# Kernel optimization log

Hardware: AMD Instinct MI355X
Metric: run time of the kernel (lower is better)

## Reference

```python
import jax, jax.numpy as jnp
import numpy as np

D_MODEL = 1024
HIDDEN = 1024
N_EXPERTS = 8
TOP_K = 2
BATCH, SEQ = 2, 2048
N_TOKENS = BATCH * SEQ


def setup_inputs() -> dict:
    key = jax.random.key(0)
    ks = jax.random.split(key, 6)
    x = jax.random.normal(ks[0], (BATCH, SEQ, D_MODEL), dtype=jnp.float32)
    expert_weights = jax.random.uniform(ks[1], (N_TOKENS, TOP_K), dtype=jnp.float32)
    expert_indices = jax.random.randint(ks[2], (N_TOKENS, TOP_K), 0, N_EXPERTS, dtype=jnp.int32)
    s_in = 1.0 / np.sqrt(D_MODEL)
    s_hid = 1.0 / np.sqrt(HIDDEN)
    w1 = jax.random.normal(ks[3], (N_EXPERTS, D_MODEL, HIDDEN), dtype=jnp.float32) * s_in
    w3 = jax.random.normal(ks[4], (N_EXPERTS, D_MODEL, HIDDEN), dtype=jnp.float32) * s_in
    w2 = jax.random.normal(ks[5], (N_EXPERTS, HIDDEN, D_MODEL), dtype=jnp.float32) * s_hid
    return {"x": x, "expert_weights": expert_weights, "expert_indices": expert_indices,
            "w1": w1, "w3": w3, "w2": w2}


def reference(x, expert_weights, expert_indices, w1, w3, w2):
    """Dropless MoE MLP (forward_once path): for each token t,
    out[t] = sum_k expert_weights[t,k] * SwiGLU_{expert_indices[t,k]}(x[t]).
    Also returns batch_size_per_expert (histogram of routed assignments).
    """
    d = x.shape[-1]
    xf = x.reshape(-1, d)                                  # [N, d]
    E = w1.shape[0]
    # combine[t, e] = sum over top-k slots routed to expert e of their weight
    onehot = jax.nn.one_hot(expert_indices, E, dtype=xf.dtype)       # [N, K, E]
    combine = jnp.einsum("nk,nke->ne", expert_weights, onehot)      # [N, E]
    out = jnp.zeros_like(xf)
    for e in range(E):  # fixed small loop over experts
        h = jax.nn.silu(xf @ w1[e]) * (xf @ w3[e])          # [N, H]
        out = out + combine[:, e:e + 1] * (h @ w2[e])       # [N, d]
    batch_size_per_expert = jnp.zeros((E,), dtype=jnp.int32).at[
        expert_indices.reshape(-1)].add(1)
    return out.reshape(x.shape), batch_size_per_expert
```

## Files before the change

### kernel.cpp

```cpp
#include <hip/hip_runtime.h>
#include <cstdint>

#define D 1024
#define N_TOKENS 4096
#define N_SLOTS 8192
#define NEXP 8
#define NKT 16
#define MAXT 80

typedef float f32x4 __attribute__((ext_vector_type(4)));
typedef __bf16 bf16x8 __attribute__((ext_vector_type(8)));
typedef __attribute__((address_space(3))) uint32_t lds_u32;
typedef __attribute__((address_space(1))) const uint32_t glb_u32;

__device__ __forceinline__ void gload_lds16(const void* g, void* l) {
  __builtin_amdgcn_global_load_lds((glb_u32*)g, (lds_u32*)l, 16, 0, 0);
}

__device__ __forceinline__ ushort f2bf(float f) {
  union { float f; uint32_t u; } c; c.f = f;
  uint32_t u = c.u;
  return (ushort)((u + 0x7FFFu + ((u >> 16) & 1u)) >> 16);
}

__device__ __forceinline__ float bf2f(ushort u) {
  union { uint32_t u; float f; } c; c.u = (uint32_t)u << 16;
  return c.f;
}

__device__ __forceinline__ bf16x8 lds_frag(const ushort* base, int row, int s) {
  return *(const bf16x8*)((const char*)base + row * 128 + ((s ^ (row & 7)) * 16));
}

__global__ void prep_k(const float* __restrict__ x, const int* __restrict__ ei,
                       const float* __restrict__ ew,
                       const float* __restrict__ w1, const float* __restrict__ w3,
                       float* __restrict__ hist_out, int* __restrict__ meta,
                       int* __restrict__ tok, int* __restrict__ smap,
                       ushort* __restrict__ Xbf, ushort* __restrict__ w13t) {
  int bid = blockIdx.x, t = threadIdx.x;
  if (bid == 0) {
    __shared__ int cmat[256][8];
    __shared__ int off[NEXP + 1];
#pragma unroll
    for (int e = 0; e < NEXP; e++) cmat[t][e] = 0;
    int base = t * 32;
#pragma unroll 4
    for (int j = 0; j < 32; j++) cmat[t][ei[base + j]]++;
    __syncthreads();
    if (t < NEXP) {
      int run = 0;
      for (int i = 0; i < 256; i++) { int v = cmat[i][t]; cmat[i][t] = run; run += v; }
      meta[8 + t] = run;
    }
    __syncthreads();
    if (t == 0) {
      int s = 0;
      for (int e = 0; e < NEXP; e++) { off[e] = s; s += meta[8 + e]; }
      off[NEXP] = s;
      int nt = 0;
      for (int e = 0; e < NEXP; e++)
        for (int r = off[e]; r < off[e + 1]; r += 128)
          if (nt < MAXT) {
            meta[16 + nt] = e;
            meta[96 + nt] = r;
            int re = off[e + 1]; if (r + 128 < re) re = r + 128;
            meta[176 + nt] = re;
            nt++;
          }
      meta[0] = nt;
      for (int e = 0; e < NEXP; e++) hist_out[e] = (float)meta[8 + e];
    }
    __syncthreads();
#pragma unroll 4
    for (int j = 0; j < 32; j++) {
      int slot = base + j;
      int e = ei[slot];
      int p = off[e] + cmat[t][e]++;
      tok[p] = slot >> 1;
      smap[slot] = p;
    }
  } else if (bid <= 256) {
    int cb = bid - 1;
    const float4* xs = (const float4*)x + (size_t)cb * 4096;
    ushort4* xd = (ushort4*)Xbf + (size_t)cb * 4096;
#pragma unroll
    for (int i = 0; i < 16; i++) {
      float4 v = xs[i * 256 + t];
      ushort4 o;
      o.x = f2bf(v.x); o.y = f2bf(v.y); o.z = f2bf(v.z); o.w = f2bf(v.w);
      xd[i * 256 + t] = o;
    }
  } else {
    int wb = bid - 257;
    int z = wb >> 8, rem = wb & 255;
    int kb = rem >> 4, nb = rem & 15;
    int which = z >> 3, e = z & 7;
    const float* src = (which == 0 ? w1 : w3) + (size_t)e * D * D;
    ushort* dst = w13t + (size_t)e * 2048 * D;
    __shared__ ushort tile[64][72];
    int k0 = kb * 64, n0 = nb * 64;
    int r = t >> 4, c = t & 15;
#pragma unroll
    for (int rep = 0; rep < 4; rep++) {
      int krow = rep * 16 + r;
      float4 v = *(const float4*)(src + (size_t)(k0 + krow) * D + n0 + c * 4);
      tile[krow][c * 4 + 0] = f2bf(v.x);
      tile[krow][c * 4 + 1] = f2bf(v.y);
      tile[krow][c * 4 + 2] = f2bf(v.z);
      tile[krow][c * 4 + 3] = f2bf(v.w);
    }
    __syncthreads();
#pragma unroll
    for (int rep = 0; rep < 4; rep++) {
      int lr = rep * 16 + r;
      int nrow = n0 + lr;
      ushort4 o;
      o.x = tile[c * 4 + 0][lr];
      o.y = tile[c * 4 + 1][lr];
      o.z = tile[c * 4 + 2][lr];
      o.w = tile[c * 4 + 3][lr];
      int crow = ((nrow >> 4) << 5) + ((which == 1) ? 16 : 0) + (nrow & 15);
      *(ushort4*)(dst + (size_t)crow * D + k0 + c * 4) = o;
    }
  }
}

#define STAGE_TILE(sAb, sBb, kb_) do {                                        \
  int kb = (kb_);                                                             \
  _Pragma("unroll")                                                           \
  for (int i = 0; i < 4; i++) {                                               \
    gload_lds16(gA + arow[i] + kb + phys[i],                                  \
                (char*)(sAb) + (i * 256 + tid) * 16);                         \
    gload_lds16(gB + (size_t)brow[i] * 2048 + kb + phys[i],                   \
                (char*)(sBb) + (i * 256 + tid) * 16);                         \
  } } while (0)

__global__ __launch_bounds__(256, 2) void gemm1_k(
    const ushort* __restrict__ Xbf, const ushort* __restrict__ W13t,
    ushort* __restrict__ H, const int* __restrict__ tok,
    const int* __restrict__ meta,
    const float* __restrict__ w2, ushort* __restrict__ W2t) {
  __shared__ ushort sA[2][128 * 64];
  __shared__ ushort sB[2][128 * 64];
  int tm = blockIdx.y;
  int tid = threadIdx.x;

  if (tm >= MAXT) {
    int e = tm - MAXT;
    const float* src = w2 + (size_t)e * D * D;
    ushort* dst = W2t + (size_t)e * D * D;
    ushort (*tile)[72] = (ushort(*)[72]) & sA[0][0];
    int kb = blockIdx.x;
    int r = tid >> 4, c = tid & 15;
    int k0 = kb * 64;
    for (int nb = 0; nb < 16; nb++) {
      int n0 = nb * 64;
      __syncthreads();
#pragma unroll
      for (int rep = 0; rep < 4; rep++) {
        int krow = rep * 16 + r;
        float4 v = *(const float4*)(src + (size_t)(k0 + krow) * D + n0 + c * 4);
        tile[krow][c * 4 + 0] = f2bf(v.x);
        tile[krow][c * 4 + 1] = f2bf(v.y);
        tile[krow][c * 4 + 2] = f2bf(v.z);
        tile[krow][c * 4 + 3] = f2bf(v.w);
      }
      __syncthreads();
#pragma unroll
      for (int rep = 0; rep < 4; rep++) {
        int lr = rep * 16 + r;
        ushort4 o;
        o.x = tile[c * 4 + 0][lr];
        o.y = tile[c * 4 + 1][lr];
        o.z = tile[c * 4 + 2][lr];
        o.w = tile[c * 4 + 3][lr];
        *(ushort4*)(dst + (size_t)(n0 + lr) * D + k0 + c * 4) = o;
      }
    }
    return;
  }
  if (tm >= meta[0]) return;

  int e = meta[16 + tm], r0 = meta[96 + tm], rend = meta[176 + tm];
  int n0i = blockIdx.x * 128;
  int lane = tid & 63, wid = tid >> 6;
  int wm = wid >> 1, wn = wid & 1;

  const char* gA = (const char*)Xbf;
  const char* gB = (const char*)(W13t + (size_t)e * 2048 * D);

  int prow = tid >> 3, pslot = tid & 7;
  size_t arow[4];
  int brow[4], phys[4];
#pragma unroll
  for (int i = 0; i < 4; i++) {
    int row = i * 32 + prow;
    int gr = r0 + row; if (gr > N_SLOTS - 1) gr = N_SLOTS - 1;
    arow[i] = (size_t)tok[gr] * 2048;
    brow[i] = n0i + row;
    phys[i] = (pslot ^ (row & 7)) * 16;
  }

  f32x4 acc[4][4] = {};

  STAGE_TILE(&sA[0][0], &sB[0][0], 0);
  int cur = 0;
  for (int kt = 0; kt < NKT; kt++) {
    if (kt + 1 < NKT) {
      STAGE_TILE(&sA[cur ^ 1][0], &sB[cur ^ 1][0], (kt + 1) * 128);
      asm volatile("s_waitcnt vmcnt(8)" ::: "memory");
    } else {
      asm volatile("s_waitcnt vmcnt(0)" ::: "memory");
    }
    __builtin_amdgcn_s_barrier();
#pragma unroll
    for (int kk = 0; kk < 2; kk++) {
      int s = kk * 4 + (lane >> 4);
      bf16x8 a[4], b[4];
#pragma unroll
      for (int mf = 0; mf < 4; mf++)
        a[mf] = lds_frag(&sA[cur][0], wm * 64 + mf * 16 + (lane & 15), s);
#pragma unroll
      for (int nf = 0; nf < 4; nf++)
        b[nf] = lds_frag(&sB[cur][0], wn * 64 + nf * 16 + (lane & 15), s);
#pragma unroll
      for (int mf = 0; mf < 4; mf++)
#pragma unroll
        for (int nf = 0; nf < 4; nf++)
          acc[mf][nf] = __builtin_amdgcn_mfma_f32_16x16x32_bf16(a[mf], b[nf], acc[mf][nf], 0, 0, 0);
    }
    __builtin_amdgcn_s_barrier();
    __builtin_amdgcn_sched_barrier(0);
    cur ^= 1;
  }

  int cb = (n0i >> 1) + wn * 32 + (lane & 15);
#pragma unroll
  for (int mf = 0; mf < 4; mf++)
#pragma unroll
    for (int v = 0; v < 4; v++) {
      int r = r0 + wm * 64 + mf * 16 + (lane >> 4) * 4 + v;
      if (r >= rend) continue;
#pragma unroll
      for (int p = 0; p < 2; p++) {
        float g = acc[mf][2 * p][v], u = acc[mf][2 * p + 1][v];
        float hv = g / (1.f + __expf(-g)) * u;
        H[(size_t)r * D + cb + p * 16] = f2bf(hv);
      }
    }
}

__global__ __launch_bounds__(256, 2) void gemm2_k(
    const ushort* __restrict__ Hm, const ushort* __restrict__ W2t,
    ushort* __restrict__ Y, const int* __restrict__ meta) {
  __shared__ ushort sA[2][128 * 64];
  __shared__ ushort sB[2][128 * 64];
  int tm = blockIdx.y;
  if (tm >= meta[0]) return;
  int e = meta[16 + tm], r0 = meta[96 + tm], rend = meta[176 + tm];
  int n0 = blockIdx.x * 128;
  int tid = threadIdx.x, lane = tid & 63, wid = tid >> 6;
  int wm = wid >> 1, wn = wid & 1;

  const char* gA = (const char*)Hm;
  const char* gB = (const char*)(W2t + (size_t)e * D * D);

  int prow = tid >> 3, pslot = tid & 7;
  size_t arow[4];
  int brow[4], phys[4];
#pragma unroll
  for (int i = 0; i < 4; i++) {
    int row = i * 32 + prow;
    int gr = r0 + row; if (gr > N_SLOTS - 1) gr = N_SLOTS - 1;
    arow[i] = (size_t)gr * 2048;
    brow[i] = n0 + row;
    phys[i] = (pslot ^ (row & 7)) * 16;
  }

  f32x4 acc[4][4] = {};

  STAGE_TILE(&sA[0][0], &sB[0][0], 0);
  int cur = 0;
  for (int kt = 0; kt < NKT; kt++) {
    if (kt + 1 < NKT) {
      STAGE_TILE(&sA[cur ^ 1][0], &sB[cur ^ 1][0], (kt + 1) * 128);
      asm volatile("s_waitcnt vmcnt(8)" ::: "memory");
    } else {
      asm volatile("s_waitcnt vmcnt(0)" ::: "memory");
    }
    __builtin_amdgcn_s_barrier();
#pragma unroll
    for (int kk = 0; kk < 2; kk++) {
      int s = kk * 4 + (lane >> 4);
      bf16x8 a[4], b[4];
#pragma unroll
      for (int mf = 0; mf < 4; mf++)
        a[mf] = lds_frag(&sA[cur][0], wm * 64 + mf * 16 + (lane & 15), s);
#pragma unroll
      for (int nf = 0; nf < 4; nf++)
        b[nf] = lds_frag(&sB[cur][0], wn * 64 + nf * 16 + (lane & 15), s);
#pragma unroll
      for (int mf = 0; mf < 4; mf++)
#pragma unroll
        for (int nf = 0; nf < 4; nf++)
          acc[mf][nf] = __builtin_amdgcn_mfma_f32_16x16x32_bf16(a[mf], b[nf], acc[mf][nf], 0, 0, 0);
    }
    __builtin_amdgcn_s_barrier();
    __builtin_amdgcn_sched_barrier(0);
    cur ^= 1;
  }

#pragma unroll
  for (int mf = 0; mf < 4; mf++)
#pragma unroll
    for (int v = 0; v < 4; v++) {
      int r = r0 + wm * 64 + mf * 16 + (lane >> 4) * 4 + v;
      if (r >= rend) continue;
#pragma unroll
      for (int nf = 0; nf < 4; nf++)
        Y[(size_t)r * D + n0 + wn * 64 + nf * 16 + (lane & 15)] = f2bf(acc[mf][nf][v]);
    }
}

__global__ void combine_k(const ushort* __restrict__ Y, const int* __restrict__ smap,
                          const float* __restrict__ ew, float* __restrict__ out) {
  int tkn = blockIdx.x * 4 + (threadIdx.x >> 6);
  int lane = threadIdx.x & 63;
  int p0 = smap[2 * tkn], p1 = smap[2 * tkn + 1];
  float w0 = ew[2 * tkn], w1 = ew[2 * tkn + 1];
  const ushort4* y0 = (const ushort4*)(Y + (size_t)p0 * D);
  const ushort4* y1 = (const ushort4*)(Y + (size_t)p1 * D);
  float4* o = (float4*)(out + (size_t)tkn * D);
#pragma unroll
  for (int j = 0; j < 4; j++) {
    int c = j * 64 + lane;
    ushort4 a = y0[c], b = y1[c];
    float4 v;
    v.x = w0 * bf2f(a.x) + w1 * bf2f(b.x);
    v.y = w0 * bf2f(a.y) + w1 * bf2f(b.y);
    v.z = w0 * bf2f(a.z) + w1 * bf2f(b.z);
    v.w = w0 * bf2f(a.w) + w1 * bf2f(b.w);
    o[c] = v;
  }
}

extern "C" void kernel_launch(void* const* d_in, const int* in_sizes, int n_in,
                              void* d_out, int out_size, void* d_ws, size_t ws_size,
                              hipStream_t stream) {
  const float* x  = (const float*)d_in[0];
  const float* ew = (const float*)d_in[1];
  const int*   ei = (const int*)d_in[2];
  const float* w1 = (const float*)d_in[3];
  const float* w3 = (const float*)d_in[4];
  const float* w2 = (const float*)d_in[5];
  float* out = (float*)d_out;

  char* ws = (char*)d_ws;
  int*    meta = (int*)ws;
  int*    tok  = (int*)(ws + 4096);
  int*    smap = (int*)(ws + 4096 + 32768);
  ushort* Xbf  = (ushort*)(ws + (1ull << 20));
  ushort* W13t = (ushort*)(ws + (9ull << 20));
  ushort* W2t  = (ushort*)(ws + (41ull << 20));
  ushort* Hm   = (ushort*)(ws + (57ull << 20));
  ushort* Ym   = (ushort*)(ws + (1ull << 20));

  prep_k<<<4353, 256, 0, stream>>>(x, ei, ew, w1, w3,
                                   out + (size_t)N_TOKENS * D, meta, tok, smap,
                                   Xbf, W13t);
  gemm1_k<<<dim3(16, MAXT + 8), 256, 0, stream>>>(Xbf, W13t, Hm, tok, meta, w2, W2t);
  gemm2_k<<<dim3(8, MAXT), 256, 0, stream>>>(Hm, W2t, Ym, meta);
  combine_k<<<N_TOKENS / 4, 256, 0, stream>>>(Ym, smap, ew, out);
}
```

Before: 136.8 us.

## Replace double-buffered GEMM staging with single buffer and raise occupancy

Both expert GEMM kernels drop the LDS double buffer and the explicit prefetch pipeline, instead loading each K tile, syncing, computing, and syncing again, with launch bounds raised to four blocks per CU. Halving LDS per block is meant to let more blocks co-reside so that other waves hide memory latency. It loses intra-block load/compute overlap and adds a second barrier per iteration. The transpose tile padding is also changed from 72 to 66.

```diff
diff --git a/kernel.cpp b/kernel.cpp
--- a/kernel.cpp
+++ b/kernel.cpp
@@ -31,6 +31,8 @@
 __device__ __forceinline__ bf16x8 lds_frag(const ushort* base, int row, int s) {
   return *(const bf16x8*)((const char*)base + row * 128 + ((s ^ (row & 7)) * 16));
 }
+
+#define TPAD 66
 
 __global__ void prep_k(const float* __restrict__ x, const int* __restrict__ ei,
                        const float* __restrict__ ew,
@@ -98,7 +100,7 @@
     int which = z >> 3, e = z & 7;
     const float* src = (which == 0 ? w1 : w3) + (size_t)e * D * D;
     ushort* dst = w13t + (size_t)e * 2048 * D;
-    __shared__ ushort tile[64][72];
+    __shared__ ushort tile[64][TPAD];
     int k0 = kb * 64, n0 = nb * 64;
     int r = t >> 4, c = t & 15;
 #pragma unroll
@@ -126,23 +128,13 @@
   }
 }
 
-#define STAGE_TILE(sAb, sBb, kb_) do {                                        \
-  int kb = (kb_);                                                             \
-  _Pragma("unroll")                                                           \
-  for (int i = 0; i < 4; i++) {                                               \
-    gload_lds16(gA + arow[i] + kb + phys[i],                                  \
-                (char*)(sAb) + (i * 256 + tid) * 16);                         \
-    gload_lds16(gB + (size_t)brow[i] * 2048 + kb + phys[i],                   \
-                (char*)(sBb) + (i * 256 + tid) * 16);                         \
-  } } while (0)
-
-__global__ __launch_bounds__(256, 2) void gemm1_k(
+__global__ __launch_bounds__(256, 4) void gemm1_k(
     const ushort* __restrict__ Xbf, const ushort* __restrict__ W13t,
     ushort* __restrict__ H, const int* __restrict__ tok,
     const int* __restrict__ meta,
     const float* __restrict__ w2, ushort* __restrict__ W2t) {
-  __shared__ ushort sA[2][128 * 64];
-  __shared__ ushort sB[2][128 * 64];
+  __shared__ ushort sA[128 * 64];
+  __shared__ ushort sB[128 * 64];
   int tm = blockIdx.y;
   int tid = threadIdx.x;
 
@@ -150,7 +142,7 @@
     int e = tm - MAXT;
     const float* src = w2 + (size_t)e * D * D;
     ushort* dst = W2t + (size_t)e * D * D;
-    ushort (*tile)[72] = (ushort(*)[72]) & sA[0][0];
+    ushort (*tile)[TPAD] = (ushort(*)[TPAD])&sA[0];
     int kb = blockIdx.x;
     int r = tid >> 4, c = tid & 15;
     int k0 = kb * 64;
@@ -187,7 +179,7 @@
   int lane = tid & 63, wid = tid >> 6;
   int wm = wid >> 1, wn = wid & 1;
 
-  const char* gA = (const char*)Xbf;
+  const char* gX = (const char*)Xbf;
   const char* gB = (const char*)(W13t + (size_t)e * 2048 * D);
 
   int prow = tid >> 3, pslot = tid & 7;
@@ -204,35 +196,32 @@
 
   f32x4 acc[4][4] = {};
 
-  STAGE_TILE(&sA[0][0], &sB[0][0], 0);
-  int cur = 0;
   for (int kt = 0; kt < NKT; kt++) {
-    if (kt + 1 < NKT) {
-      STAGE_TILE(&sA[cur ^ 1][0], &sB[cur ^ 1][0], (kt + 1) * 128);
-      asm volatile("s_waitcnt vmcnt(8)" ::: "memory");
-    } else {
-      asm volatile("s_waitcnt vmcnt(0)" ::: "memory");
-    }
-    __builtin_amdgcn_s_barrier();
+    int kb = kt * 128;
+#pragma unroll
+    for (int i = 0; i < 4; i++) {
+      gload_lds16(gX + arow[i] + kb + phys[i], (char*)sA + (i * 256 + tid) * 16);
+      gload_lds16(gB + (size_t)brow[i] * 2048 + kb + phys[i],
+                  (char*)sB + (i * 256 + tid) * 16);
+    }
+    __syncthreads();
 #pragma unroll
     for (int kk = 0; kk < 2; kk++) {
       int s = kk * 4 + (lane >> 4);
       bf16x8 a[4], b[4];
 #pragma unroll
       for (int mf = 0; mf < 4; mf++)
-        a[mf] = lds_frag(&sA[cur][0], wm * 64 + mf * 16 + (lane & 15), s);
+        a[mf] = lds_frag(sA, wm * 64 + mf * 16 + (lane & 15), s);
 #pragma unroll
       for (int nf = 0; nf < 4; nf++)
-        b[nf] = lds_frag(&sB[cur][0], wn * 64 + nf * 16 + (lane & 15), s);
+        b[nf] = lds_frag(sB, wn * 64 + nf * 16 + (lane & 15), s);
 #pragma unroll
       for (int mf = 0; mf < 4; mf++)
 #pragma unroll
         for (int nf = 0; nf < 4; nf++)
           acc[mf][nf] = __builtin_amdgcn_mfma_f32_16x16x32_bf16(a[mf], b[nf], acc[mf][nf], 0, 0, 0);
     }
-    __builtin_amdgcn_s_barrier();
-    __builtin_amdgcn_sched_barrier(0);
-    cur ^= 1;
+    __syncthreads();
   }
 
   int cb = (n0i >> 1) + wn * 32 + (lane & 15);
@@ -251,11 +240,11 @@
     }
 }
 
-__global__ __launch_bounds__(256, 2) void gemm2_k(
+__global__ __launch_bounds__(256, 4) void gemm2_k(
     const ushort* __restrict__ Hm, const ushort* __restrict__ W2t,
     ushort* __restrict__ Y, const int* __restrict__ meta) {
-  __shared__ ushort sA[2][128 * 64];
-  __shared__ ushort sB[2][128 * 64];
+  __shared__ ushort sA[128 * 64];
+  __shared__ ushort sB[128 * 64];
   int tm = blockIdx.y;
   if (tm >= meta[0]) return;
   int e = meta[16 + tm], r0 = meta[96 + tm], rend = meta[176 + tm];
@@ -263,7 +252,7 @@
   int tid = threadIdx.x, lane = tid & 63, wid = tid >> 6;
   int wm = wid >> 1, wn = wid & 1;
 
-  const char* gA = (const char*)Hm;
+  const char* gH = (const char*)Hm;
   const char* gB = (const char*)(W2t + (size_t)e * D * D);
 
   int prow = tid >> 3, pslot = tid & 7;
@@ -280,35 +269,32 @@
 
   f32x4 acc[4][4] = {};
 
-  STAGE_TILE(&sA[0][0], &sB[0][0], 0);
-  int cur = 0;
   for (int kt = 0; kt < NKT; kt++) {
-    if (kt + 1 < NKT) {
-      STAGE_TILE(&sA[cur ^ 1][0], &sB[cur ^ 1][0], (kt + 1) * 128);
-      asm volatile("s_waitcnt vmcnt(8)" ::: "memory");
-    } else {
-      asm volatile("s_waitcnt vmcnt(0)" ::: "memory");
-    }
-    __builtin_amdgcn_s_barrier();
+    int kb = kt * 128;
+#pragma unroll
+    for (int i = 0; i < 4; i++) {
+      gload_lds16(gH + arow[i] + kb + phys[i], (char*)sA + (i * 256 + tid) * 16);
+      gload_lds16(gB + (size_t)brow[i] * 2048 + kb + phys[i],
+                  (char*)sB + (i * 256 + tid) * 16);
+    }
+    __syncthreads();
 #pragma unroll
     for (int kk = 0; kk < 2; kk++) {
       int s = kk * 4 + (lane >> 4);
       bf16x8 a[4], b[4];
 #pragma unroll
       for (int mf = 0; mf < 4; mf++)
-        a[mf] = lds_frag(&sA[cur][0], wm * 64 + mf * 16 + (lane & 15), s);
+        a[mf] = lds_frag(sA, wm * 64 + mf * 16 + (lane & 15), s);
 #pragma unroll
       for (int nf = 0; nf < 4; nf++)
-        b[nf] = lds_frag(&sB[cur][0], wn * 64 + nf * 16 + (lane & 15), s);
+        b[nf] = lds_frag(sB, wn * 64 + nf * 16 + (lane & 15), s);
 #pragma unroll
       for (int mf = 0; mf < 4; mf++)
 #pragma unroll
         for (int nf = 0; nf < 4; nf++)
           acc[mf][nf] = __builtin_amdgcn_mfma_f32_16x16x32_bf16(a[mf], b[nf], acc[mf][nf], 0, 0, 0);
     }
-    __builtin_amdgcn_s_barrier();
-    __builtin_amdgcn_sched_barrier(0);
-    cur ^= 1;
+    __syncthreads();
   }
 
 #pragma unroll
```

New measurement: 116.0 us. -15.2%, faster.
